# Optimization experiments

Hardware: AMD Instinct MI355X
Metric: run time of the kernel (lower is better)

## Reference

```python
import jax, jax.numpy as jnp
import numpy as np

EPS = 1e-5  # BatchNorm eps (torch default)

def _bn(x, gamma, beta):
    # training-mode BatchNorm over the edge/node (leading) axis, biased var
    mean = x.mean(axis=0, keepdims=True)
    var = x.var(axis=0, keepdims=True)
    return (x - mean) * jax.lax.rsqrt(var + EPS) * gamma + beta

def _silu(x):
    return x * jax.nn.sigmoid(x)

def setup_inputs() -> dict:
    N, E, H, NH = 50000, 800000, 128, 4
    HD = H // NH
    key = jax.random.key(0)
    ks = jax.random.split(key, 8)
    x = jax.random.normal(ks[0], (N, H), dtype=jnp.float32)
    weight = jax.random.uniform(ks[1], (N, 1), dtype=jnp.float32)  # positive fraction weights
    src = jax.random.randint(ks[2], (E,), 0, N)
    dst = jax.random.randint(ks[3], (E,), 0, N)
    # f: Linear(2H, 1) + BN(1)
    Wf = jax.random.normal(ks[4], (2 * H, 1), dtype=jnp.float32) * 0.05
    bf = jnp.zeros((1,), jnp.float32)
    f_gamma = jnp.ones((1,), jnp.float32)
    f_beta = jnp.zeros((1,), jnp.float32)
    # g: NH heads of Linear(2H, HD) + BN(HD), stacked on leading head axis
    Wg = jax.random.normal(ks[5], (NH, 2 * H, HD), dtype=jnp.float32) * 0.05
    bg = jnp.zeros((NH, HD), jnp.float32)
    g_gamma = jnp.ones((NH, HD), jnp.float32)
    g_beta = jnp.zeros((NH, HD), jnp.float32)
    # bn_nodes: BN(H)
    n_gamma = jnp.ones((H,), jnp.float32)
    n_beta = jnp.zeros((H,), jnp.float32)
    return dict(x=x, weight=weight, src=src, dst=dst, Wf=Wf, bf=bf,
                f_gamma=f_gamma, f_beta=f_beta, Wg=Wg, bg=bg,
                g_gamma=g_gamma, g_beta=g_beta, n_gamma=n_gamma, n_beta=n_beta)

def reference(x, weight, src, dst, Wf, bf, f_gamma, f_beta, Wg, bg, g_gamma, g_beta, n_gamma, n_beta):
    N = x.shape[0]
    E = src.shape[0]
    # per-edge concat of src/dst node features: [E, 2H]
    hihj = jnp.concatenate([x[src], x[dst]], axis=-1)
    # attention logit f(hihj) = SiLU(BN(Linear)) then exp: [E, 1]
    exp_e = jnp.exp(_silu(_bn(hihj @ Wf + bf, f_gamma, f_beta)))
    # weighted softmax-like normalization over incoming edges of each dst node
    we = weight[src] * exp_e                                   # [E, 1]
    sum_w_exp = jax.ops.segment_sum(we, dst, num_segments=N)   # [N, 1]
    a = we / sum_w_exp[dst]                                    # [E, 1]
    # multi-head message: a_ij * SiLU(BN(Linear_h(hihj))) per head, concat
    z = jnp.einsum('ed,hdk->ehk', hihj, Wg) + bg               # [E, NH, HD]
    z = _silu(_bn(z, g_gamma, g_beta))
    msg = (a[:, :, None] * z).reshape(E, -1)                   # [E, H]
    h = jax.ops.segment_sum(msg, dst, num_segments=N)          # [N, H]
    out = _bn(h, n_gamma, n_beta) + x                          # residual
    return out
```

## Files before the change

kernel.cpp:

```cpp
#include <hip/hip_runtime.h>
#include <hip/hip_bf16.h>
#include <math.h>

#define HDIM 128
#define PAD 64
#define CSTR 16
typedef unsigned short ushort_t;
typedef unsigned int uint_t;
typedef __attribute__((ext_vector_type(8))) short bf16x8;
typedef __attribute__((ext_vector_type(4))) float f32x4;
typedef __attribute__((ext_vector_type(2))) float v2f;

__device__ __forceinline__ float wave_allreduce(float v){
  #pragma unroll
  for (int o = 1; o < 64; o <<= 1) v += __shfl_xor(v, o);
  return v;
}

__device__ __forceinline__ ushort_t f2bf(float f){
  uint_t u = __float_as_uint(f);
  uint_t r = (u + 0x7fffu + ((u >> 16) & 1u)) >> 16;
  return (ushort_t)r;
}

__device__ __forceinline__ v2f bf2(uint_t u){
  v2f r;
  r.x = __uint_as_float(u << 16);
  r.y = __uint_as_float(u & 0xffff0000u);
  return r;
}

__global__ __launch_bounds__(128) void k_wpack(const float* __restrict__ Wg,
    const float* __restrict__ Wf, ushort_t* __restrict__ W2t,
    int* __restrict__ cnt, int C){
  int b = blockIdx.x;
  int k = threadIdx.x;
  if (b < 272){
    float val;
    if (b < 128)       val = Wg[(size_t)(b >> 5) * 8192 + k * 32 + (b & 31)];
    else if (b < 256){ int c2 = b - 128;
                       val = Wg[(size_t)(c2 >> 5) * 8192 + (k + 128) * 32 + (c2 & 31)]; }
    else if (b == 256) val = Wf[k];
    else if (b == 257) val = Wf[128 + k];
    else               val = 0.f;
    W2t[(size_t)b * 128 + k] = f2bf(val);
  } else {
    int i = (b - 272) * 128 + k;
    if (i < C) cnt[i] = 0;
  }
}

__global__ __launch_bounds__(256) void k_gemmfill(const float* __restrict__ x,
    const ushort_t* __restrict__ W2t, const float* __restrict__ weight,
    ushort_t* __restrict__ Pb, ushort_t* __restrict__ Qb,
    float* __restrict__ v, float2* __restrict__ uw2,
    const int* __restrict__ src, const int* __restrict__ dst,
    int* __restrict__ cnt, int* __restrict__ es,
    int N, int E, int GB){
  if ((int)blockIdx.x < GB){
    int wid = __builtin_amdgcn_readfirstlane(threadIdx.x >> 6);
    int lane = threadIdx.x & 63;
    int quad = lane >> 4, col = lane & 15;
    int strip = blockIdx.x * 2 + (wid >> 1);
    int half = wid & 1;
    int n_base = strip * 16;
    if (n_base >= N) return;
    int tbeg = half * 8;
    int ntile = half ? 9 : 8;
    f32x4 acc[9];
    #pragma unroll
    for (int t = 0; t < 9; ++t) acc[t] = (f32x4){0.f, 0.f, 0.f, 0.f};
    int row = n_base + col;
    int rowc = row < N ? row : N - 1;
    const float* xr = x + (size_t)rowc * HDIM + quad * 8;
    #pragma unroll
    for (int kk = 0; kk < 4; ++kk){
      float4 a0 = *(const float4*)(xr + kk * 32);
      float4 a1 = *(const float4*)(xr + kk * 32 + 4);
      bf16x8 af;
      af[0] = (short)f2bf(a0.x); af[1] = (short)f2bf(a0.y);
      af[2] = (short)f2bf(a0.z); af[3] = (short)f2bf(a0.w);
      af[4] = (short)f2bf(a1.x); af[5] = (short)f2bf(a1.y);
      af[6] = (short)f2bf(a1.z); af[7] = (short)f2bf(a1.w);
      const ushort_t* wb = W2t + (size_t)(tbeg * 16) * 128 + (size_t)col * 128 + kk * 32 + quad * 8;
      #pragma unroll
      for (int t = 0; t < 9; ++t){
        if (t < ntile){
          bf16x8 bfr = *(const bf16x8*)(wb + (size_t)t * 16 * 128);
          acc[t] = __builtin_amdgcn_mfma_f32_16x16x32_bf16(af, bfr, acc[t], 0, 0, 0);
        }
      }
    }
    #pragma unroll
    for (int t = 0; t < 8; ++t){
      int ct = tbeg + t;
      int c = ct * 16 + col;
      #pragma unroll
      for (int r = 0; r < 4; ++r){
        int n = n_base + quad * 4 + r;
        if (n < N){
          ushort_t valb = f2bf(acc[t][r]);
          if (c < 128) Pb[(size_t)n * HDIM + c] = valb;
          else         Qb[(size_t)n * HDIM + (c - 128)] = valb;
        }
      }
    }
    if (half){
      #pragma unroll
      for (int r = 0; r < 4; ++r){
        int n = n_base + quad * 4 + r;
        if (n < N){
          float val = acc[8][r];
          if (col == 0)      uw2[n] = make_float2(val, weight[n]);
          else if (col == 1) v[n] = val;
        }
      }
    }
  } else {
    int bi = blockIdx.x - GB;
    int part = (int)blockIdx.x & 7;
    int nch = (gridDim.x - GB) >> 3;
    int chunk = bi >> 3;
    int Npp = (N + 7) >> 3;
    int lo = part * Npp;
    int hi = lo + Npp; if (hi > N) hi = N;
    int stride = nch * 256;
    int e = chunk * 256 + threadIdx.x;
#define FILL1(d, s) if ((d) >= lo && (d) < hi){ \
    int c = atomicAdd(&cnt[(size_t)(d) * CSTR], 1); \
    if (c < PAD) es[(size_t)(d) * PAD + c] = (s); }
    for (; e + 7 * stride < E; e += 8 * stride){
      int d0 = dst[e],            d1 = dst[e + stride];
      int d2 = dst[e + 2*stride], d3 = dst[e + 3*stride];
      int d4 = dst[e + 4*stride], d5 = dst[e + 5*stride];
      int d6 = dst[e + 6*stride], d7 = dst[e + 7*stride];
      int s0 = src[e],            s1 = src[e + stride];
      int s2 = src[e + 2*stride], s3 = src[e + 3*stride];
      int s4 = src[e + 4*stride], s5 = src[e + 5*stride];
      int s6 = src[e + 6*stride], s7 = src[e + 7*stride];
      FILL1(d0, s0) FILL1(d1, s1) FILL1(d2, s2) FILL1(d3, s3)
      FILL1(d4, s4) FILL1(d5, s5) FILL1(d6, s6) FILL1(d7, s7)
    }
    for (; e < E; e += stride){
      int d = dst[e];
      FILL1(d, src[e])
    }
#undef FILL1
  }
}

#define SH8(sjv,jj,S) \
  int S##0=__shfl(sjv,(jj)),   S##1=__shfl(sjv,(jj)+1), S##2=__shfl(sjv,(jj)+2), S##3=__shfl(sjv,(jj)+3), \
      S##4=__shfl(sjv,(jj)+4), S##5=__shfl(sjv,(jj)+5), S##6=__shfl(sjv,(jj)+6), S##7=__shfl(sjv,(jj)+7);
#define LD8(S,P) \
  uint_t P##0=Pu[(size_t)S##0*64+lane], P##1=Pu[(size_t)S##1*64+lane], \
         P##2=Pu[(size_t)S##2*64+lane], P##3=Pu[(size_t)S##3*64+lane], \
         P##4=Pu[(size_t)S##4*64+lane], P##5=Pu[(size_t)S##5*64+lane], \
         P##6=Pu[(size_t)S##6*64+lane], P##7=Pu[(size_t)S##7*64+lane];
#define SH4(sjv,jj,S) \
  int S##0=__shfl(sjv,(jj)),   S##1=__shfl(sjv,(jj)+1), S##2=__shfl(sjv,(jj)+2), S##3=__shfl(sjv,(jj)+3);
#define LD4(S,P) \
  uint_t P##0=Pu[(size_t)S##0*64+lane], P##1=Pu[(size_t)S##1*64+lane], \
         P##2=Pu[(size_t)S##2*64+lane], P##3=Pu[(size_t)S##3*64+lane];

__global__ __launch_bounds__(256) void k_gstats(const ushort_t* __restrict__ Pb,
    const ushort_t* __restrict__ Qb, const float* __restrict__ v,
    const float2* __restrict__ uw2, const int* __restrict__ es,
    const int* __restrict__ cnt, float* __restrict__ pstatG, int N){
  int lane = threadIdx.x & 63;
  int wid = __builtin_amdgcn_readfirstlane(threadIdx.x >> 6);
  int part = (int)blockIdx.x & 7;
  int Npp = (N + 7) >> 3;
  int lo = part * Npp;
  int hi = lo + Npp; if (hi > N) hi = N;
  int stp = (gridDim.x >> 3) << 2;
  const uint_t* Pu = (const uint_t*)Pb;
  const uint_t* Qu = (const uint_t*)Qb;
  v2f gs = {0.f,0.f}, gq = {0.f,0.f};
  float fs = 0.f, fq = 0.f;
  int n0 = lo + ((blockIdx.x >> 3) << 2) + wid;
  int n1 = n0 + stp;
  int dnA=0,sjA=0; uint_t qAu=0; float vA=0.f;
  int dnB=0,sjB=0; uint_t qBu=0; float vB=0.f;
  if (n0 < hi){ dnA=cnt[(size_t)n0*CSTR]; sjA=es[(size_t)n0*PAD+lane];
                qAu=Qu[(size_t)n0*64+lane]; vA=v[n0]; }
  if (n1 < hi){ dnB=cnt[(size_t)n1*CSTR]; sjB=es[(size_t)n1*PAD+lane];
                qBu=Qu[(size_t)n1*64+lane]; vB=v[n1]; }
#define GST(p,Sv,Qv) { v2f y=bf2(p); Sv+=y; Qv.x=fmaf(y.x,y.x,Qv.x); Qv.y=fmaf(y.y,y.y,Qv.y); }
#define GED8(P,Sv,Qv) GST(P##0,Sv,Qv) GST(P##1,Sv,Qv) GST(P##2,Sv,Qv) GST(P##3,Sv,Qv) \
                      GST(P##4,Sv,Qv) GST(P##5,Sv,Qv) GST(P##6,Sv,Qv) GST(P##7,Sv,Qv)
#define GED4(P,Sv,Qv) GST(P##0,Sv,Qv) GST(P##1,Sv,Qv) GST(P##2,Sv,Qv) GST(P##3,Sv,Qv)
  while (n0 < hi){
    int m0 = n0 + 2*stp, m1 = n1 + 2*stp;
    int dnC=0,sjC=0; uint_t qCu=0; float vC=0.f;
    int dnD=0,sjD=0; uint_t qDu=0; float vD=0.f;
    if (m0 < hi){ dnC=cnt[(size_t)m0*CSTR]; sjC=es[(size_t)m0*PAD+lane];
                  qCu=Qu[(size_t)m0*64+lane]; vC=v[m0]; }
    if (m1 < hi){ dnD=cnt[(size_t)m1*CSTR]; sjD=es[(size_t)m1*PAD+lane];
                  qDu=Qu[(size_t)m1*64+lane]; vD=v[m1]; }
    int dA = dnA < PAD ? dnA : PAD;
    int dB = (n1 < hi) ? (dnB < PAD ? dnB : PAD) : 0;
    if (lane < dA){ float2 uw = uw2[sjA]; float t = uw.x + vA; fs += t; fq = fmaf(t,t,fq); }
    if (lane < dB){ float2 uw = uw2[sjB]; float t = uw.x + vB; fs += t; fq = fmaf(t,t,fq); }
    v2f qa = bf2(qAu), qb = bf2(qBu);
    v2f SnA={0.f,0.f}, SSA={0.f,0.f}, SnB={0.f,0.f}, SSB={0.f,0.f};
    int j0 = 0, j1 = 0;
    for (; j0 + 7 < dA && j1 + 7 < dB; j0 += 8, j1 += 8){
      SH8(sjA,j0,xa) SH8(sjB,j1,xb)
      LD8(xa,pa) LD8(xb,pb)
      GED8(pa,SnA,SSA) GED8(pb,SnB,SSB)
    }
    for (; j0 + 7 < dA; j0 += 8){ SH8(sjA,j0,xa) LD8(xa,pa) GED8(pa,SnA,SSA) }
    for (; j0 + 3 < dA; j0 += 4){ SH4(sjA,j0,xa) LD4(xa,pa) GED4(pa,SnA,SSA) }
    for (; j0 < dA; ++j0){ int s0=__shfl(sjA,j0); uint_t p0=Pu[(size_t)s0*64+lane]; GST(p0,SnA,SSA) }
    for (; j1 + 7 < dB; j1 += 8){ SH8(sjB,j1,xb) LD8(xb,pb) GED8(pb,SnB,SSB) }
    for (; j1 + 3 < dB; j1 += 4){ SH4(sjB,j1,xb) LD4(xb,pb) GED4(pb,SnB,SSB) }
    for (; j1 < dB; ++j1){ int s0=__shfl(sjB,j1); uint_t p0=Pu[(size_t)s0*64+lane]; GST(p0,SnB,SSB) }
    float dAf = (float)dA, dBf = (float)dB;
    gs.x += SnA.x + SnB.x + dAf*qa.x + dBf*qb.x;
    gs.y += SnA.y + SnB.y + dAf*qa.y + dBf*qb.y;
    gq.x += SSA.x + SSB.x + qa.x*fmaf(dAf,qa.x,2.f*SnA.x) + qb.x*fmaf(dBf,qb.x,2.f*SnB.x);
    gq.y += SSA.y + SSB.y + qa.y*fmaf(dAf,qa.y,2.f*SnA.y) + qb.y*fmaf(dBf,qb.y,2.f*SnB.y);
    n0 = m0; n1 = m1;
    dnA=dnC; sjA=sjC; qAu=qCu; vA=vC;
    dnB=dnD; sjB=sjD; qBu=qDu; vB=vD;
  }
#undef GST
#undef GED8
#undef GED4
  fs = wave_allreduce(fs); fq = wave_allreduce(fq);
  __shared__ float red[4][258];
  red[wid][2*lane]       = gs.x; red[wid][2*lane+1]   = gs.y;
  red[wid][128+2*lane]   = gq.x; red[wid][129+2*lane] = gq.y;
  if (lane == 0){ red[wid][256] = fs; red[wid][257] = fq; }
  __syncthreads();
  for (int c = threadIdx.x; c < 258; c += 256)
    pstatG[(size_t)blockIdx.x * 258 + c] = red[0][c] + red[1][c] + red[2][c] + red[3][c];
}

__global__ __launch_bounds__(256) void k_redfin1(const float* __restrict__ pstatG,
    int NB, const float* __restrict__ g_gamma, const float* __restrict__ g_beta,
    const float* __restrict__ f_gamma, const float* __restrict__ f_beta,
    float* __restrict__ fin, long long E){
  int j = blockIdx.x;
  int c1 = (j < 128) ? j : 256;
  int c2 = (j < 128) ? 128 + j : 257;
  double s1 = 0, s2 = 0;
  for (int b = threadIdx.x; b < NB; b += 256){
    const float* pb = pstatG + (size_t)b * 258;
    s1 += (double)pb[c1]; s2 += (double)pb[c2];
  }
  __shared__ double m1[256], m2[256];
  m1[threadIdx.x] = s1; m2[threadIdx.x] = s2;
  __syncthreads();
  for (int o = 128; o; o >>= 1){
    if (threadIdx.x < o){ m1[threadIdx.x] += m1[threadIdx.x + o];
                          m2[threadIdx.x] += m2[threadIdx.x + o]; }
    __syncthreads();
  }
  if (threadIdx.x == 0){
    double m = m1[0] / (double)E;
    double var = m2[0] / (double)E - m * m;
    if (j < 128){
      float sc = (float)((double)g_gamma[j] / sqrt(var + 1e-5));
      fin[2 + j] = sc; fin[130 + j] = g_beta[j] - (float)m * sc;
    } else {
      float sc = (float)((double)f_gamma[0] / sqrt(var + 1e-5));
      fin[0] = sc; fin[1] = f_beta[0] - (float)m * sc;
    }
  }
}

__global__ __launch_bounds__(256) void k_msg(const ushort_t* __restrict__ Pb,
    const ushort_t* __restrict__ Qb, const float* __restrict__ v,
    const float2* __restrict__ uw2, const int* __restrict__ es,
    const int* __restrict__ cnt, const float* __restrict__ fin,
    float* __restrict__ h, float* __restrict__ pstatH, int N){
  int lane = threadIdx.x & 63;
  int wid = __builtin_amdgcn_readfirstlane(threadIdx.x >> 6);
  int part = (int)blockIdx.x & 7;
  int Npp = (N + 7) >> 3;
  int lo = part * Npp;
  int hi = lo + Npp; if (hi > N) hi = N;
  int stp = (gridDim.x >> 3) << 2;
  const uint_t* Pu = (const uint_t*)Pb;
  const uint_t* Qu = (const uint_t*)Qb;
  float fsc = fin[0], fsh = fin[1];
  v2f gsc = {fin[2 + 2*lane], fin[3 + 2*lane]};
  v2f gsh = {fin[130 + 2*lane], fin[131 + 2*lane]};
  v2f hs = {0.f,0.f}, hq = {0.f,0.f};
  int n0 = lo + ((blockIdx.x >> 3) << 2) + wid;
  int n1 = n0 + stp;
  int dnA=0,sjA=0; uint_t qAu=0; float vA=0.f;
  int dnB=0,sjB=0; uint_t qBu=0; float vB=0.f;
  if (n0 < hi){ dnA=cnt[(size_t)n0*CSTR]; sjA=es[(size_t)n0*PAD+lane];
                qAu=Qu[(size_t)n0*64+lane]; vA=v[n0]; }
  if (n1 < hi){ dnB=cnt[(size_t)n1*CSTR]; sjB=es[(size_t)n1*PAD+lane];
                qBu=Qu[(size_t)n1*64+lane]; vB=v[n1]; }
#define EDGE(p,a,qv,av) { v2f y = (bf2(p) + qv) * gsc + gsh; \
      float e0 = __expf(-y.x), e1 = __expf(-y.y); \
      float d0 = 1.f + e0, d1 = 1.f + e1; \
      float r = __builtin_amdgcn_rcpf(d0 * d1) * (a); \
      av.x = fmaf(y.x * d1, r, av.x); av.y = fmaf(y.y * d0, r, av.y); }
#define ASH8(wjv,jj,A) \
  float A##0=__shfl(wjv,(jj)),   A##1=__shfl(wjv,(jj)+1), A##2=__shfl(wjv,(jj)+2), A##3=__shfl(wjv,(jj)+3), \
        A##4=__shfl(wjv,(jj)+4), A##5=__shfl(wjv,(jj)+5), A##6=__shfl(wjv,(jj)+6), A##7=__shfl(wjv,(jj)+7);
#define ASH4(wjv,jj,A) \
  float A##0=__shfl(wjv,(jj)),   A##1=__shfl(wjv,(jj)+1), A##2=__shfl(wjv,(jj)+2), A##3=__shfl(wjv,(jj)+3);
#define MED8(P,A,qv,av) EDGE(P##0,A##0,qv,av) EDGE(P##1,A##1,qv,av) EDGE(P##2,A##2,qv,av) EDGE(P##3,A##3,qv,av) \
                        EDGE(P##4,A##4,qv,av) EDGE(P##5,A##5,qv,av) EDGE(P##6,A##6,qv,av) EDGE(P##7,A##7,qv,av)
#define MED4(P,A,qv,av) EDGE(P##0,A##0,qv,av) EDGE(P##1,A##1,qv,av) EDGE(P##2,A##2,qv,av) EDGE(P##3,A##3,qv,av)
  while (n0 < hi){
    int m0 = n0 + 2*stp, m1 = n1 + 2*stp;
    int dnC=0,sjC=0; uint_t qCu=0; float vC=0.f;
    int dnD=0,sjD=0; uint_t qDu=0; float vD=0.f;
    if (m0 < hi){ dnC=cnt[(size_t)m0*CSTR]; sjC=es[(size_t)m0*PAD+lane];
                  qCu=Qu[(size_t)m0*64+lane]; vC=v[m0]; }
    if (m1 < hi){ dnD=cnt[(size_t)m1*CSTR]; sjD=es[(size_t)m1*PAD+lane];
                  qDu=Qu[(size_t)m1*64+lane]; vD=v[m1]; }
    int dA = dnA < PAD ? dnA : PAD;
    int dB = (n1 < hi) ? (dnB < PAD ? dnB : PAD) : 0;
    float wjA = 0.f, wjB = 0.f;
    if (lane < dA){ float2 uw = uw2[sjA];
      float tt = fmaf(uw.x + vA, fsc, fsh);
      float sl = tt * __builtin_amdgcn_rcpf(1.f + __expf(-tt));
      wjA = uw.y * __expf(sl); }
    if (lane < dB){ float2 uw = uw2[sjB];
      float tt = fmaf(uw.x + vB, fsc, fsh);
      float sl = tt * __builtin_amdgcn_rcpf(1.f + __expf(-tt));
      wjB = uw.y * __expf(sl); }
    v2f qa = bf2(qAu), qb = bf2(qBu);
    v2f accA = {0.f,0.f}, accB = {0.f,0.f};
    int j0 = 0, j1 = 0;
    for (; j0 + 7 < dA && j1 + 7 < dB; j0 += 8, j1 += 8){
      SH8(sjA,j0,xa) SH8(sjB,j1,xb)
      ASH8(wjA,j0,aa) ASH8(wjB,j1,ab)
      LD8(xa,pa) LD8(xb,pb)
      MED8(pa,aa,qa,accA) MED8(pb,ab,qb,accB)
    }
    for (; j0 + 7 < dA; j0 += 8){ SH8(sjA,j0,xa) ASH8(wjA,j0,aa) LD8(xa,pa) MED8(pa,aa,qa,accA) }
    for (; j0 + 3 < dA; j0 += 4){ SH4(sjA,j0,xa) ASH4(wjA,j0,aa) LD4(xa,pa) MED4(pa,aa,qa,accA) }
    for (; j0 < dA; ++j0){ int s0=__shfl(sjA,j0); float a0=__shfl(wjA,j0);
                           uint_t p0=Pu[(size_t)s0*64+lane]; EDGE(p0,a0,qa,accA) }
    for (; j1 + 7 < dB; j1 += 8){ SH8(sjB,j1,xb) ASH8(wjB,j1,ab) LD8(xb,pb) MED8(pb,ab,qb,accB) }
    for (; j1 + 3 < dB; j1 += 4){ SH4(sjB,j1,xb) ASH4(wjB,j1,ab) LD4(xb,pb) MED4(pb,ab,qb,accB) }
    for (; j1 < dB; ++j1){ int s0=__shfl(sjB,j1); float a0=__shfl(wjB,j1);
                           uint_t p0=Pu[(size_t)s0*64+lane]; EDGE(p0,a0,qb,accB) }
    float swA = wjA, swB = wjB;
    #pragma unroll
    for (int o = 1; o < 64; o <<= 1){ swA += __shfl_xor(swA, o); swB += __shfl_xor(swB, o); }
    float rsA = (dA > 0) ? (1.f / swA) : 0.f;
    float rsB = (dB > 0) ? (1.f / swB) : 0.f;
    accA.x *= rsA; accA.y *= rsA;
    accB.x *= rsB; accB.y *= rsB;
    *(float2*)&h[(size_t)n0 * 128 + 2*lane] = make_float2(accA.x, accA.y);
    hs += accA; hq += accA * accA;
    if (n1 < hi){
      *(float2*)&h[(size_t)n1 * 128 + 2*lane] = make_float2(accB.x, accB.y);
      hs += accB; hq += accB * accB;
    }
    n0 = m0; n1 = m1;
    dnA=dnC; sjA=sjC; qAu=qCu; vA=vC;
    dnB=dnD; sjB=sjD; qBu=qDu; vB=vD;
  }
#undef EDGE
#undef ASH8
#undef ASH4
#undef MED8
#undef MED4
  __shared__ float red[4][256];
  red[wid][2*lane]       = hs.x; red[wid][2*lane+1]   = hs.y;
  red[wid][128+2*lane]   = hq.x; red[wid][129+2*lane] = hq.y;
  __syncthreads();
  int c = threadIdx.x;
  pstatH[(size_t)blockIdx.x * 256 + c] = red[0][c] + red[1][c] + red[2][c] + red[3][c];
}

__global__ __launch_bounds__(256) void k_redfin2(const float* __restrict__ pstatH,
    int NB, const float* __restrict__ n_gamma, const float* __restrict__ n_beta,
    float* __restrict__ fin, int N){
  int j = blockIdx.x;
  double s1 = 0, s2 = 0;
  for (int b = threadIdx.x; b < NB; b += 256){
    const float* pb = pstatH + (size_t)b * 256;
    s1 += (double)pb[j]; s2 += (double)pb[128 + j];
  }
  __shared__ double m1[256], m2[256];
  m1[threadIdx.x] = s1; m2[threadIdx.x] = s2;
  __syncthreads();
  for (int o = 128; o; o >>= 1){
    if (threadIdx.x < o){ m1[threadIdx.x] += m1[threadIdx.x + o];
                          m2[threadIdx.x] += m2[threadIdx.x + o]; }
    __syncthreads();
  }
  if (threadIdx.x == 0){
    double m = m1[0] / (double)N;
    double var = m2[0] / (double)N - m * m;
    float sc = (float)((double)n_gamma[j] / sqrt(var + 1e-5));
    fin[258 + j] = sc; fin[386 + j] = n_beta[j] - (float)m * sc;
  }
}

__global__ __launch_bounds__(256) void k_out(const float* __restrict__ h,
    const float* __restrict__ x, const float* __restrict__ fin,
    float* __restrict__ out, int total4){
  int i = blockIdx.x * 256 + threadIdx.x;
  if (i >= total4) return;
  const float4* h4 = (const float4*)h; const float4* x4 = (const float4*)x;
  float4 hv = h4[i], xv = x4[i];
  int c = (i * 4) & 127;
  float4 o;
  o.x = fmaf(hv.x, fin[258 + c],     fin[386 + c])     + xv.x;
  o.y = fmaf(hv.y, fin[258 + c + 1], fin[386 + c + 1]) + xv.y;
  o.z = fmaf(hv.z, fin[258 + c + 2], fin[386 + c + 2]) + xv.z;
  o.w = fmaf(hv.w, fin[258 + c + 3], fin[386 + c + 3]) + xv.w;
  ((float4*)out)[i] = o;
}

extern "C" void kernel_launch(void* const* d_in, const int* in_sizes, int n_in,
                              void* d_out, int out_size, void* d_ws, size_t ws_size,
                              hipStream_t stream){
  const float* x       = (const float*)d_in[0];
  const float* weight  = (const float*)d_in[1];
  const int*   src     = (const int*)d_in[2];
  const int*   dst     = (const int*)d_in[3];
  const float* Wf      = (const float*)d_in[4];
  const float* f_gamma = (const float*)d_in[6];
  const float* f_beta  = (const float*)d_in[7];
  const float* Wg      = (const float*)d_in[8];
  const float* g_gamma = (const float*)d_in[10];
  const float* g_beta  = (const float*)d_in[11];
  const float* n_gamma = (const float*)d_in[12];
  const float* n_beta  = (const float*)d_in[13];
  float* out = (float*)d_out;

  int N = in_sizes[0] / HDIM;
  int E = in_sizes[2];

  char* ws = (char*)d_ws;
  size_t off = 0;
  auto alloc = [&](size_t bytes)->char*{
    char* p = ws + off; off = (off + bytes + 255) & ~(size_t)255; return p;
  };
  ushort_t* Pb    = (ushort_t*)alloc((size_t)N * HDIM * 2);
  ushort_t* Qb    = (ushort_t*)alloc((size_t)N * HDIM * 2);
  float* h        = (float*)alloc((size_t)N * HDIM * 4);
  float* v        = (float*)alloc((size_t)N * 4);
  float2* uw2     = (float2*)alloc((size_t)N * 8);
  int* es         = (int*)alloc((size_t)N * PAD * 4);
  ushort_t* W2t   = (ushort_t*)alloc((size_t)272 * 128 * 2);
  int* cnt        = (int*)alloc((size_t)N * CSTR * 4);
  const int NWB = 2048;
  const int NB  = NWB;
  float*  pstatG = (float*)alloc((size_t)NB * 258 * 4);
  float*  pstatH = (float*)alloc((size_t)NB * 256 * 4);
  float*  fin    = (float*)alloc(514 * 4);

  int GB = (N + 31) / 32;
  const int FB = 1024;
  int CT = N * CSTR;

  k_wpack   <<<272 + (CT + 127) / 128, 128, 0, stream>>>(Wg, Wf, W2t, cnt, CT);
  k_gemmfill<<<GB + FB, 256, 0, stream>>>(x, W2t, weight, Pb, Qb, v, uw2,
                                          src, dst, cnt, es, N, E, GB);
  k_gstats  <<<NWB, 256, 0, stream>>>(Pb, Qb, v, uw2, es, cnt, pstatG, N);
  k_redfin1 <<<129, 256, 0, stream>>>(pstatG, NB, g_gamma, g_beta, f_gamma, f_beta, fin, (long long)E);
  k_msg     <<<NWB, 256, 0, stream>>>(Pb, Qb, v, uw2, es, cnt, fin, h, pstatH, N);
  k_redfin2 <<<128, 256, 0, stream>>>(pstatH, NB, n_gamma, n_beta, fin, N);
  k_out     <<<(N * HDIM / 4 + 255) / 256, 256, 0, stream>>>(h, x, fin, out, N * HDIM / 4);
}
```

Measured before the change: 280.2 us.

## Stage x and GEMM outputs through LDS for coalesced loads and stores

The node GEMM in k_gemmfill now loads each block's 32 rows of x cooperatively into LDS as bf16 with an XOR swizzle, then reads MFMA A fragments from LDS. Previously each wave reread strided float4s from global memory. Weights are repacked into a tiled layout so each k-chunk of B fragments is contiguous. Results are staged in LDS and written to Pb/Qb as full 16-byte row segments instead of scattered 2-byte stores. This adds about 25KB of LDS to every block, including the edge-fill blocks, which may reduce occupancy for the atomic fill path.

```diff
diff --git a/kernel.cpp b/kernel.cpp
--- a/kernel.cpp
+++ b/kernel.cpp
@@ -31,7 +31,7 @@
 }
 
 __global__ __launch_bounds__(128) void k_wpack(const float* __restrict__ Wg,
-    const float* __restrict__ Wf, ushort_t* __restrict__ W2t,
+    const float* __restrict__ Wf, ushort_t* __restrict__ W3,
     int* __restrict__ cnt, int C){
   int b = blockIdx.x;
   int k = threadIdx.x;
@@ -43,7 +43,8 @@
     else if (b == 256) val = Wf[k];
     else if (b == 257) val = Wf[128 + k];
     else               val = 0.f;
-    W2t[(size_t)b * 128 + k] = f2bf(val);
+    int idx = (((b >> 4) * 4 + (k >> 5)) * 16 + (b & 15)) * 32 + (k & 31);
+    W3[idx] = f2bf(val);
   } else {
     int i = (b - 272) * 128 + k;
     if (i < C) cnt[i] = 0;
@@ -51,42 +52,49 @@
 }
 
 __global__ __launch_bounds__(256) void k_gemmfill(const float* __restrict__ x,
-    const ushort_t* __restrict__ W2t, const float* __restrict__ weight,
+    const ushort_t* __restrict__ W3, const float* __restrict__ weight,
     ushort_t* __restrict__ Pb, ushort_t* __restrict__ Qb,
     float* __restrict__ v, float2* __restrict__ uw2,
     const int* __restrict__ src, const int* __restrict__ dst,
     int* __restrict__ cnt, int* __restrict__ es,
     int N, int E, int GB){
+  __shared__ ushort_t xl[32 * 128];
+  __shared__ ushort_t cl[32 * 264];
   if ((int)blockIdx.x < GB){
-    int wid = __builtin_amdgcn_readfirstlane(threadIdx.x >> 6);
-    int lane = threadIdx.x & 63;
+    int tid = threadIdx.x;
+    int n_base = blockIdx.x * 32;
+    #pragma unroll
+    for (int i = 0; i < 4; ++i){
+      int cidx = i * 256 + tid;
+      int row = cidx >> 5, ch = cidx & 31;
+      int rowc = n_base + row; rowc = rowc < N ? rowc : N - 1;
+      float4 a = *(const float4*)(x + (size_t)rowc * HDIM + ch * 4);
+      uint_t lo = (uint_t)f2bf(a.x) | ((uint_t)f2bf(a.y) << 16);
+      uint_t hi = (uint_t)f2bf(a.z) | ((uint_t)f2bf(a.w) << 16);
+      int bo = (row * 256 + ch * 8) ^ ((row & 7) << 4);
+      *(uint2*)((char*)xl + bo) = make_uint2(lo, hi);
+    }
+    __syncthreads();
+    int wid = __builtin_amdgcn_readfirstlane(tid >> 6);
+    int lane = tid & 63;
     int quad = lane >> 4, col = lane & 15;
-    int strip = blockIdx.x * 2 + (wid >> 1);
+    int strip = wid >> 1;
     int half = wid & 1;
-    int n_base = strip * 16;
-    if (n_base >= N) return;
     int tbeg = half * 8;
     int ntile = half ? 9 : 8;
     f32x4 acc[9];
     #pragma unroll
     for (int t = 0; t < 9; ++t) acc[t] = (f32x4){0.f, 0.f, 0.f, 0.f};
-    int row = n_base + col;
-    int rowc = row < N ? row : N - 1;
-    const float* xr = x + (size_t)rowc * HDIM + quad * 8;
+    int arow = strip * 16 + col;
     #pragma unroll
     for (int kk = 0; kk < 4; ++kk){
-      float4 a0 = *(const float4*)(xr + kk * 32);
-      float4 a1 = *(const float4*)(xr + kk * 32 + 4);
-      bf16x8 af;
-      af[0] = (short)f2bf(a0.x); af[1] = (short)f2bf(a0.y);
-      af[2] = (short)f2bf(a0.z); af[3] = (short)f2bf(a0.w);
-      af[4] = (short)f2bf(a1.x); af[5] = (short)f2bf(a1.y);
-      af[6] = (short)f2bf(a1.z); af[7] = (short)f2bf(a1.w);
-      const ushort_t* wb = W2t + (size_t)(tbeg * 16) * 128 + (size_t)col * 128 + kk * 32 + quad * 8;
+      int abyte = (arow * 256 + kk * 64 + quad * 16) ^ ((col & 7) << 4);
+      bf16x8 af = *(const bf16x8*)((char*)xl + abyte);
+      const ushort_t* wb = W3 + (size_t)(tbeg * 4 + kk) * 512 + col * 32 + quad * 8;
       #pragma unroll
       for (int t = 0; t < 9; ++t){
         if (t < ntile){
-          bf16x8 bfr = *(const bf16x8*)(wb + (size_t)t * 16 * 128);
+          bf16x8 bfr = *(const bf16x8*)(wb + (size_t)t * 2048);
           acc[t] = __builtin_amdgcn_mfma_f32_16x16x32_bf16(af, bfr, acc[t], 0, 0, 0);
         }
       }
@@ -94,26 +102,40 @@
     #pragma unroll
     for (int t = 0; t < 8; ++t){
       int ct = tbeg + t;
-      int c = ct * 16 + col;
       #pragma unroll
       for (int r = 0; r < 4; ++r){
-        int n = n_base + quad * 4 + r;
-        if (n < N){
-          ushort_t valb = f2bf(acc[t][r]);
-          if (c < 128) Pb[(size_t)n * HDIM + c] = valb;
-          else         Qb[(size_t)n * HDIM + (c - 128)] = valb;
-        }
+        int lr = strip * 16 + quad * 4 + r;
+        cl[lr * 264 + ct * 16 + col] = f2bf(acc[t][r]);
       }
     }
     if (half){
       #pragma unroll
       for (int r = 0; r < 4; ++r){
-        int n = n_base + quad * 4 + r;
+        int n = n_base + strip * 16 + quad * 4 + r;
         if (n < N){
           float val = acc[8][r];
           if (col == 0)      uw2[n] = make_float2(val, weight[n]);
           else if (col == 1) v[n] = val;
         }
+      }
+    }
+    __syncthreads();
+    int row = tid >> 3, seg = tid & 7;
+    int n = n_base + row;
+    if (n < N){
+      const ushort_t* s = cl + row * 264 + seg * 32;
+      uint4 w0 = *(const uint4*)(s);
+      uint4 w1 = *(const uint4*)(s + 8);
+      uint4 w2 = *(const uint4*)(s + 16);
+      uint4 w3v = *(const uint4*)(s + 24);
+      if (seg < 4){
+        ushort_t* dp = Pb + (size_t)n * HDIM + seg * 32;
+        *(uint4*)(dp) = w0; *(uint4*)(dp + 8) = w1;
+        *(uint4*)(dp + 16) = w2; *(uint4*)(dp + 24) = w3v;
+      } else {
+        ushort_t* dp = Qb + (size_t)n * HDIM + (seg - 4) * 32;
+        *(uint4*)(dp) = w0; *(uint4*)(dp + 8) = w1;
+        *(uint4*)(dp + 16) = w2; *(uint4*)(dp + 24) = w3v;
       }
     }
   } else {
@@ -448,7 +470,7 @@
   float* v        = (float*)alloc((size_t)N * 4);
   float2* uw2     = (float2*)alloc((size_t)N * 8);
   int* es         = (int*)alloc((size_t)N * PAD * 4);
-  ushort_t* W2t   = (ushort_t*)alloc((size_t)272 * 128 * 2);
+  ushort_t* W3    = (ushort_t*)alloc((size_t)272 * 128 * 2);
   int* cnt        = (int*)alloc((size_t)N * CSTR * 4);
   const int NWB = 2048;
   const int NB  = NWB;
@@ -460,8 +482,8 @@
   const int FB = 1024;
   int CT = N * CSTR;
 
-  k_wpack   <<<272 + (CT + 127) / 128, 128, 0, stream>>>(Wg, Wf, W2t, cnt, CT);
-  k_gemmfill<<<GB + FB, 256, 0, stream>>>(x, W2t, weight, Pb, Qb, v, uw2,
+  k_wpack   <<<272 + (CT + 127) / 128, 128, 0, stream>>>(Wg, Wf, W3, cnt, CT);
+  k_gemmfill<<<GB + FB, 256, 0, stream>>>(x, W3, weight, Pb, Qb, v, uw2,
                                           src, dst, cnt, es, N, E, GB);
   k_gstats  <<<NWB, 256, 0, stream>>>(Pb, Qb, v, uw2, es, cnt, pstatG, N);
   k_redfin1 <<<129, 256, 0, stream>>>(pstatG, NB, g_gamma, g_beta, f_gamma, f_beta, fin, (long long)E);
```

Measured after the change: 275.7 us. No clear change (-1.6%).
